# Performance work log

Measured on AMD Instinct MI355X. Metric: run time of the kernel, lower is better.

## Reference

```python
import jax, jax.numpy as jnp
import numpy as np

HEAD_DIM = 1024
SCALE = HEAD_DIM ** -0.25  # qk_scale defaults to exponent -0.25


def setup_inputs() -> dict:
    key = jax.random.key(0)
    ks = jax.random.split(key, 6)
    B_s, B_q, C = 4096, 4096, 1024
    return {
        "query": jax.random.normal(ks[0], (B_q, C), dtype=jnp.float32),
        "s": jax.random.normal(ks[1], (B_s, C), dtype=jnp.float32),
        "TG_prompt": jax.random.normal(ks[2], (B_s, C), dtype=jnp.float32),
        "W_qkv": jax.random.normal(ks[3], (3 * HEAD_DIM, C), dtype=jnp.float32) * (C ** -0.5),
        "W_proj_s": jax.random.normal(ks[4], (HEAD_DIM, HEAD_DIM), dtype=jnp.float32) * (HEAD_DIM ** -0.5),
        "W_proj_q": jax.random.normal(ks[5], (HEAD_DIM, HEAD_DIM), dtype=jnp.float32) * (HEAD_DIM ** -0.5),
    }


def reference(query, s, TG_prompt, W_qkv, W_proj_s, W_proj_q):
    B_s = s.shape[0]
    t = s + TG_prompt                       # [B_s, C]
    c = jnp.concatenate([t, query], axis=0)  # [B, C], B = B_s + B_q
    x = c @ W_qkv.T                          # [B, 3*head_dim]
    q, k, v = jnp.split(x, 3, axis=-1)       # each [B, head_dim]
    # separate sqrt-scale on q and k, then full [B, B] scores
    attn = jax.nn.softmax((q * SCALE) @ (k.T * SCALE), axis=-1)
    attn_cq = attn[:B_s, B_s:]               # [B_s, B_q]
    attn_qc = attn[B_s:, :B_s]               # [B_q, B_s]
    # matmul against raw query / s (NOT v), then per-branch projection
    x_s = (attn_cq @ query) @ W_proj_s.T     # [B_s, head_dim]
    x_q = (attn_qc @ s) @ W_proj_q.T         # [B_q, head_dim]
    return (x_s, x_q)
```

## Files before the change

kernel.cpp:

```cpp
#include <hip/hip_runtime.h>


typedef unsigned short u16;
typedef __bf16 bf16x8 __attribute__((ext_vector_type(8)));
typedef float f32x4 __attribute__((ext_vector_type(4)));
typedef unsigned short u16x8 __attribute__((ext_vector_type(8)));

#define DEVI static __device__ __forceinline__

DEVI u16 f2b(float f) {
  unsigned int u = __float_as_uint(f);
  u += 0x7fffu + ((u >> 16) & 1u);
  return (u16)(u >> 16);
}

DEVI float exp2_hw(float x) {
  float r;
  asm("v_exp_f32 %0, %1" : "=v"(r) : "v"(x));
  return r;
}

__global__ void prep_all(const float* __restrict__ query, const float* __restrict__ s,
                         const float* __restrict__ tg, const float* __restrict__ w0,
                         const float* __restrict__ w1, const float* __restrict__ w2,
                         u16* __restrict__ cB, u16* __restrict__ sBf,
                         u16* __restrict__ o0, u16* __restrict__ o1,
                         u16* __restrict__ o2, float* __restrict__ rowsum) {
  int b = blockIdx.x;
  if (b >= 6144) {
    int i = (b - 6144) * 1024 + (int)threadIdx.x * 4;
    rowsum[i] = 0.f; rowsum[i + 1] = 0.f; rowsum[i + 2] = 0.f; rowsum[i + 3] = 0.f;
    return;
  }
  if (b < 4096) {
    int base = (b * 256 + threadIdx.x) << 3;
    int row = base >> 10;
    u16x8 o;
    if (row < 4096) {
      float4 a0 = *(const float4*)(s + base);
      float4 a1 = *(const float4*)(s + base + 4);
      float4 b0 = *(const float4*)(tg + base);
      float4 b1 = *(const float4*)(tg + base + 4);
      u16x8 os;
      os[0] = f2b(a0.x); os[1] = f2b(a0.y); os[2] = f2b(a0.z); os[3] = f2b(a0.w);
      os[4] = f2b(a1.x); os[5] = f2b(a1.y); os[6] = f2b(a1.z); os[7] = f2b(a1.w);
      *(u16x8*)(sBf + base) = os;
      o[0] = f2b(a0.x + b0.x); o[1] = f2b(a0.y + b0.y);
      o[2] = f2b(a0.z + b0.z); o[3] = f2b(a0.w + b0.w);
      o[4] = f2b(a1.x + b1.x); o[5] = f2b(a1.y + b1.y);
      o[6] = f2b(a1.z + b1.z); o[7] = f2b(a1.w + b1.w);
    } else {
      int qb = base - 4096 * 1024;
      float4 a0 = *(const float4*)(query + qb);
      float4 a1 = *(const float4*)(query + qb + 4);
      o[0] = f2b(a0.x); o[1] = f2b(a0.y); o[2] = f2b(a0.z); o[3] = f2b(a0.w);
      o[4] = f2b(a1.x); o[5] = f2b(a1.y); o[6] = f2b(a1.z); o[7] = f2b(a1.w);
    }
    *(u16x8*)(cB + base) = o;
  } else {
    const float* in; u16* out; int lb;
    if (b < 5120)      { in = w0; out = o0; lb = b - 4096; }
    else if (b < 5632) { in = w1; out = o1; lb = b - 5120; }
    else               { in = w2; out = o2; lb = b - 5632; }
    int base = (lb * 256 + threadIdx.x) << 3;
    float4 a0 = *(const float4*)(in + base);
    float4 a1 = *(const float4*)(in + base + 4);
    u16x8 o;
    o[0] = f2b(a0.x); o[1] = f2b(a0.y); o[2] = f2b(a0.z); o[3] = f2b(a0.w);
    o[4] = f2b(a1.x); o[5] = f2b(a1.y); o[6] = f2b(a1.z); o[7] = f2b(a1.w);
    *(u16x8*)(out + base) = o;
  }
}

struct KLoopOut { f32x4 acc[4][4]; };

DEVI void kloop(const u16* Ab, const u16* Bb, int lda, int ldb, int K,
                u16* sA, u16* sB, int tid, int wr, int wc, f32x4 (&acc)[4][4]) {
  const int lane = tid & 63;
  const int ar = lane & 15;
  const int sr = tid >> 3;
  const int scL = (tid & 7) << 3;
  const int scG = ((tid & 7) ^ (sr & 7)) << 3;

  const int l7 = lane & 7, l16 = lane >> 4;
  const int p0b = (l16 ^ l7) << 4;
  const int offA0 = (wr + ar) * 128 + p0b;
  const int offB0 = (wc + ar) * 128 + p0b;
  const char* sAc = (const char*)sA;
  const char* sBc = (const char*)sB;

  for (int k0 = 0; k0 < K; k0 += 64) {
#pragma unroll
    for (int it = 0; it < 4; ++it) {
      int r = it * 64 + sr;
      __builtin_amdgcn_global_load_lds(
          (__attribute__((address_space(1))) void*)(Ab + (size_t)r * lda + k0 + scG),
          (__attribute__((address_space(3))) void*)(sA + r * 64 + scL), 16, 0, 0);
    }
#pragma unroll
    for (int it = 0; it < 2; ++it) {
      int r = it * 64 + sr;
      __builtin_amdgcn_global_load_lds(
          (__attribute__((address_space(1))) void*)(Bb + (size_t)r * ldb + k0 + scG),
          (__attribute__((address_space(3))) void*)(sB + r * 64 + scL), 16, 0, 0);
    }
    __syncthreads();
#pragma unroll
    for (int half = 0; half < 2; ++half) {
      const int px = half ? 64 : 0;
      bf16x8 af[4], bfr[4];
#pragma unroll
      for (int t = 0; t < 4; ++t)
        af[t] = *(const bf16x8*)(sAc + ((offA0 ^ px) + t * 2048));
#pragma unroll
      for (int t = 0; t < 4; ++t)
        bfr[t] = *(const bf16x8*)(sBc + ((offB0 ^ px) + t * 2048));
#pragma unroll
      for (int tm = 0; tm < 4; ++tm)
#pragma unroll
        for (int tn = 0; tn < 4; ++tn)
          acc[tm][tn] = __builtin_amdgcn_mfma_f32_16x16x32_bf16(
              af[tm], bfr[tn], acc[tm][tn], 0, 0, 0);
    }
    __syncthreads();
  }
}

__global__ __launch_bounds__(512)
void gemm_qkv(const u16* __restrict__ cB, const u16* __restrict__ WqkB,
              u16* __restrict__ qks,
              const u16* __restrict__ WpsB, const u16* __restrict__ WpqB,
              const u16* __restrict__ qBf, const u16* __restrict__ sBf,
              u16* __restrict__ VsT, u16* __restrict__ VqT,
              float sq, float sk) {
  __shared__ __align__(16) u16 sA[256 * 64];
  __shared__ __align__(16) u16 sB[128 * 64];
  const int b = blockIdx.x;
  const u16* Ap; const u16* Bp; u16* op;
  int bx, by, ldc;
  bool proj;
  if (b < 512) {
    proj = true;  bx = b & 15; by = b >> 4;
    Ap = cB; Bp = WqkB; op = qks; ldc = 2048;
  } else {
    proj = false;
    int b2 = b - 512;
    int z = b2 >> 7, rem = b2 & 127;
    bx = rem & 31; by = rem >> 5;
    Ap = z ? WpqB : WpsB; Bp = z ? sBf : qBf; op = z ? VqT : VsT; ldc = 4096;
  }
  const int tid = threadIdx.x;
  const int lane = tid & 63;
  const int wave = tid >> 6;
  const int wr = (wave >> 1) * 64;
  const int wc = (wave & 1) * 64;

  f32x4 acc[4][4];
#pragma unroll
  for (int i = 0; i < 4; ++i)
#pragma unroll
    for (int j = 0; j < 4; ++j) acc[i][j] = f32x4{0.f, 0.f, 0.f, 0.f};

  kloop(Ap + (size_t)(by * 256) * 1024, Bp + (size_t)(bx * 128) * 1024,
        1024, 1024, 1024, sA, sB, tid, wr, wc, acc);

  const int qr = (lane >> 4) * 4;
  const int qc = lane & 15;
#pragma unroll
  for (int tm = 0; tm < 4; ++tm)
#pragma unroll
    for (int r = 0; r < 4; ++r) {
      int row = by * 256 + wr + tm * 16 + qr + r;
#pragma unroll
      for (int tn = 0; tn < 4; ++tn) {
        int col = bx * 128 + wc + tn * 16 + qc;
        float sc = proj ? ((col < 1024) ? sq : sk) : 1.0f;
        op[(size_t)row * ldc + col] = f2b(acc[tm][tn][r] * sc);
      }
    }
}

template <int EPI>
__global__ __launch_bounds__(512)
void gemm_bt(const u16* __restrict__ A, const u16* __restrict__ A1,
             const u16* __restrict__ B, const u16* __restrict__ B1,
             int lda, int ldb, int K, int ldc,
             float* __restrict__ outf, float* __restrict__ outf1,
             const float* __restrict__ rs, const float* __restrict__ rs1,
             u16* __restrict__ Pcq, u16* __restrict__ Pqc,
             float* __restrict__ rowsum) {
  __shared__ __align__(16) u16 sA[256 * 64];
  __shared__ __align__(16) u16 sB[128 * 64];
  const int tid = threadIdx.x;
  const int lane = tid & 63;
  const int wave = tid >> 6;
  const int wr = (wave >> 1) * 64;
  const int wc = (wave & 1) * 64;
  const int by = blockIdx.y, bx = blockIdx.x;
  const int z = blockIdx.z;

  f32x4 acc[4][4];
#pragma unroll
  for (int i = 0; i < 4; ++i)
#pragma unroll
    for (int j = 0; j < 4; ++j) acc[i][j] = f32x4{0.f, 0.f, 0.f, 0.f};

  kloop((z ? A1 : A) + (size_t)(by * 256) * lda,
        (z ? B1 : B) + (size_t)(bx * 128) * ldb,
        lda, ldb, K, sA, sB, tid, wr, wc, acc);

  const int qr = (lane >> 4) * 4;
  const int qc = lane & 15;

  if constexpr (EPI == 1) {
    const bool top = (by < 16);
    const bool left = (bx < 32);
    u16* pdst = nullptr;
    if (top && !left) pdst = Pcq;
    if (!top && left) pdst = Pqc;
    const int growb = by * 256 + wr;
    const int rbase = growb - (top ? 0 : 4096);
    const int cbase = bx * 128 + wc - (left ? 0 : 4096);
#pragma unroll
    for (int tm = 0; tm < 4; ++tm) {
      float e[4][4];
      float rsum[4] = {0.f, 0.f, 0.f, 0.f};
#pragma unroll
      for (int tn = 0; tn < 4; ++tn)
#pragma unroll
        for (int r = 0; r < 4; ++r) {
          e[tn][r] = exp2_hw(acc[tm][tn][r]);
          rsum[r] += e[tn][r];
        }
#pragma unroll
      for (int r = 0; r < 4; ++r) {
        float v = rsum[r];
        v += __shfl_xor(v, 1);
        v += __shfl_xor(v, 2);
        v += __shfl_xor(v, 4);
        v += __shfl_xor(v, 8);
        if ((lane & 15) == 0)
          atomicAdd(&rowsum[growb + tm * 16 + qr + r], v);
      }
      if (pdst) {
#pragma unroll
        for (int tn = 0; tn < 4; ++tn)
#pragma unroll
          for (int r = 0; r < 4; ++r) {
            int row = rbase + tm * 16 + qr + r;
            pdst[(size_t)row * 4096 + cbase + tn * 16 + qc] = f2b(e[tn][r]);
          }
      }
    }
  } else {
    float* of = z ? outf1 : outf;
    const float* rsz = z ? rs1 : rs;
#pragma unroll
    for (int tm = 0; tm < 4; ++tm)
#pragma unroll
      for (int r = 0; r < 4; ++r) {
        int row = by * 256 + wr + tm * 16 + qr + r;
        float inv = 1.0f / rsz[row];
#pragma unroll
        for (int tn = 0; tn < 4; ++tn) {
          int col = bx * 128 + wc + tn * 16 + qc;
          of[(size_t)row * ldc + col] = acc[tm][tn][r] * inv;
        }
      }
  }
}


extern "C" void kernel_launch(void* const* d_in, const int* in_sizes, int n_in,
                              void* d_out, int out_size, void* d_ws, size_t ws_size,
                              hipStream_t stream) {
  (void)in_sizes; (void)n_in; (void)out_size; (void)ws_size;
  const float* query = (const float*)d_in[0];
  const float* s     = (const float*)d_in[1];
  const float* tg    = (const float*)d_in[2];
  const float* Wqkv  = (const float*)d_in[3];
  const float* Wps   = (const float*)d_in[4];
  const float* Wpq   = (const float*)d_in[5];
  float* out = (float*)d_out;

  char* ws = (char*)d_ws;
  u16* cB     = (u16*)ws; ws += (size_t)8192 * 1024 * 2;
  u16* sBf    = (u16*)ws; ws += (size_t)4096 * 1024 * 2;
  u16* qks    = (u16*)ws; ws += (size_t)8192 * 2048 * 2;
  u16* WqkB   = (u16*)ws; ws += (size_t)2048 * 1024 * 2;
  u16* WpsB   = (u16*)ws; ws += (size_t)1024 * 1024 * 2;
  u16* WpqB   = (u16*)ws; ws += (size_t)1024 * 1024 * 2;
  u16* VsT    = (u16*)ws; ws += (size_t)1024 * 4096 * 2;
  u16* VqT    = (u16*)ws; ws += (size_t)1024 * 4096 * 2;
  u16* Pcq    = (u16*)ws; ws += (size_t)4096 * 4096 * 2;
  u16* Pqc    = (u16*)ws; ws += (size_t)4096 * 4096 * 2;
  float* rowsum = (float*)ws;

  const u16* qBf = cB + (size_t)4096 * 1024;

  const float SCALE = 0.17677669529663687f;
  const float LOG2E = 1.4426950408889634f;

  prep_all<<<6152, 256, 0, stream>>>(query, s, tg, Wqkv, Wps, Wpq,
                                     cB, sBf, WqkB, WpsB, WpqB, rowsum);
  gemm_qkv<<<768, 512, 0, stream>>>(cB, WqkB, qks, WpsB, WpqB, qBf, sBf,
                                    VsT, VqT, SCALE * LOG2E, SCALE);
  gemm_bt<1><<<dim3(64, 32), 512, 0, stream>>>(
      qks, nullptr, qks + 1024, nullptr, 2048, 2048, 1024, 0,
      nullptr, nullptr, nullptr, nullptr, Pcq, Pqc, rowsum);
  gemm_bt<4><<<dim3(8, 16, 2), 512, 0, stream>>>(
      Pcq, Pqc, VsT, VqT, 4096, 4096, 4096, 1024,
      out, out + (size_t)4096 * 1024, rowsum, rowsum + 4096,
      nullptr, nullptr, nullptr);
}
```

Measured before the change: 431.0 us.

## Replace score GEMM with 256x256-tile double-buffered kernel using direct-to-LDS loads

Adds a dedicated scores kernel that uses 256x256 output tiles per block instead of 256x128. Tiles are staged through global_load_lds into double-buffered LDS, with MFMA groups split into quarters separated by barriers and raised wave priority. This raises arithmetic intensity and overlaps the next K-tile's loads with compute for the dominant 8192x8192x1024 GEMM. In exchange it doubles the accumulator registers per thread (acc[8][4]), uses 128KB of LDS, and halves the grid, which may lower occupancy.

```diff
diff --git a/kernel.cpp b/kernel.cpp
--- a/kernel.cpp
+++ b/kernel.cpp
@@ -72,8 +72,6 @@
   }
 }
 
-struct KLoopOut { f32x4 acc[4][4]; };
-
 DEVI void kloop(const u16* Ab, const u16* Bb, int lda, int ldb, int K,
                 u16* sA, u16* sB, int tid, int wr, int wc, f32x4 (&acc)[4][4]) {
   const int lane = tid & 63;
@@ -180,6 +178,167 @@
     }
 }
 
+__global__ __launch_bounds__(512)
+void gemm_sc(const u16* __restrict__ A, const u16* __restrict__ B,
+             u16* __restrict__ Pcq, u16* __restrict__ Pqc,
+             float* __restrict__ rowsum) {
+  __shared__ __align__(16) u16 lds[2][2][256 * 64];
+  const int tid = threadIdx.x;
+  const int lane = tid & 63;
+  const int wave = tid >> 6;
+  const int wm = wave >> 2;
+  const int wn = wave & 3;
+  const int bx = blockIdx.x, by = blockIdx.y;
+
+  const int sr = tid >> 3;
+  const int scL = (tid & 7) << 3;
+  const int scG = ((tid & 7) ^ (sr & 7)) << 3;
+
+  const int l7 = lane & 7, l16 = lane >> 4;
+  const int ar = lane & 15;
+  const int p0b = (l16 ^ l7) << 4;
+  const int offA0 = (wm * 128 + ar) * 128 + p0b;
+  const int offB0 = (wn * 64 + ar) * 128 + p0b;
+
+  const u16* Ag = A + (size_t)(by * 256) * 2048;
+  const u16* Bg = B + (size_t)(bx * 256) * 2048;
+
+#define STAGE_SC(DST, K0)                                                     \
+  _Pragma("unroll")                                                           \
+  for (int it_ = 0; it_ < 4; ++it_) {                                         \
+    const int r_ = it_ * 64 + sr;                                             \
+    __builtin_amdgcn_global_load_lds(                                         \
+        (__attribute__((address_space(1))) void*)(Ag + (size_t)r_ * 2048 + (K0) + scG), \
+        (__attribute__((address_space(3))) void*)(&lds[DST][0][r_ * 64 + scL]), 16, 0, 0); \
+    __builtin_amdgcn_global_load_lds(                                         \
+        (__attribute__((address_space(1))) void*)(Bg + (size_t)r_ * 2048 + (K0) + scG), \
+        (__attribute__((address_space(3))) void*)(&lds[DST][1][r_ * 64 + scL]), 16, 0, 0); \
+  }
+
+#define MFMA_Q(MQ, NQ)                                                        \
+  _Pragma("unroll")                                                           \
+  for (int tm_ = 0; tm_ < 4; ++tm_) {                                         \
+    _Pragma("unroll")                                                         \
+    for (int tn_ = 0; tn_ < 2; ++tn_) {                                       \
+      _Pragma("unroll")                                                       \
+      for (int kh_ = 0; kh_ < 2; ++kh_)                                       \
+        acc[(MQ) * 4 + tm_][(NQ) * 2 + tn_] =                                 \
+            __builtin_amdgcn_mfma_f32_16x16x32_bf16(                          \
+                af[tm_][kh_], bfr[NQ][tn_][kh_],                              \
+                acc[(MQ) * 4 + tm_][(NQ) * 2 + tn_], 0, 0, 0);                \
+    }                                                                         \
+  }
+
+  f32x4 acc[8][4];
+#pragma unroll
+  for (int i = 0; i < 8; ++i)
+#pragma unroll
+    for (int j = 0; j < 4; ++j) acc[i][j] = f32x4{0.f, 0.f, 0.f, 0.f};
+
+  STAGE_SC(0, 0)
+
+#pragma unroll 1
+  for (int kt = 0; kt < 16; ++kt) {
+    const int cur = kt & 1;
+    const char* sAc = (const char*)lds[cur][0];
+    const char* sBc = (const char*)lds[cur][1];
+
+    if (kt < 15) {
+      STAGE_SC(cur ^ 1, (kt + 1) * 64)
+      asm volatile("s_waitcnt vmcnt(8)\n\ts_barrier" ::: "memory");
+    } else {
+      asm volatile("s_waitcnt vmcnt(0)\n\ts_barrier" ::: "memory");
+    }
+
+    bf16x8 af[4][2];
+    bf16x8 bfr[2][2][2];
+#pragma unroll
+    for (int t_ = 0; t_ < 4; ++t_) {
+      af[t_][0] = *(const bf16x8*)(sAc + (offA0 + t_ * 2048));
+      af[t_][1] = *(const bf16x8*)(sAc + ((offA0 + t_ * 2048) ^ 64));
+    }
+#pragma unroll
+    for (int nq_ = 0; nq_ < 2; ++nq_)
+#pragma unroll
+      for (int t_ = 0; t_ < 2; ++t_) {
+        bfr[nq_][t_][0] = *(const bf16x8*)(sBc + (offB0 + nq_ * 4096 + t_ * 2048));
+        bfr[nq_][t_][1] = *(const bf16x8*)(sBc + ((offB0 + nq_ * 4096 + t_ * 2048) ^ 64));
+      }
+    asm volatile("s_waitcnt lgkmcnt(0)" ::: "memory");
+    __builtin_amdgcn_sched_barrier(0);
+    __builtin_amdgcn_s_setprio(1);
+    MFMA_Q(0, 0)
+    __builtin_amdgcn_s_setprio(0);
+    asm volatile("s_barrier" ::: "memory");
+
+    __builtin_amdgcn_s_setprio(1);
+    MFMA_Q(0, 1)
+    __builtin_amdgcn_s_setprio(0);
+    asm volatile("s_barrier" ::: "memory");
+
+#pragma unroll
+    for (int t_ = 0; t_ < 4; ++t_) {
+      af[t_][0] = *(const bf16x8*)(sAc + (offA0 + 8192 + t_ * 2048));
+      af[t_][1] = *(const bf16x8*)(sAc + ((offA0 + 8192 + t_ * 2048) ^ 64));
+    }
+    asm volatile("s_waitcnt lgkmcnt(0)" ::: "memory");
+    __builtin_amdgcn_sched_barrier(0);
+    __builtin_amdgcn_s_setprio(1);
+    MFMA_Q(1, 0)
+    __builtin_amdgcn_s_setprio(0);
+    asm volatile("s_barrier" ::: "memory");
+
+    __builtin_amdgcn_s_setprio(1);
+    MFMA_Q(1, 1)
+    __builtin_amdgcn_s_setprio(0);
+    asm volatile("s_barrier" ::: "memory");
+  }
+
+  const int qr = (lane >> 4) * 4;
+  const int qc = lane & 15;
+  const bool top = (by < 16);
+  const bool left = (bx < 16);
+  u16* pdst = nullptr;
+  if (top && !left) pdst = Pcq;
+  if (!top && left) pdst = Pqc;
+  const int growb = by * 256 + wm * 128;
+  const int rbase = growb - (top ? 0 : 4096);
+  const int cbase = bx * 256 + wn * 64 - (left ? 0 : 4096);
+#pragma unroll
+  for (int i = 0; i < 8; ++i) {
+    float e[4][4];
+    float rsum[4] = {0.f, 0.f, 0.f, 0.f};
+#pragma unroll
+    for (int j = 0; j < 4; ++j)
+#pragma unroll
+      for (int r = 0; r < 4; ++r) {
+        e[j][r] = exp2_hw(acc[i][j][r]);
+        rsum[r] += e[j][r];
+      }
+#pragma unroll
+    for (int r = 0; r < 4; ++r) {
+      float v = rsum[r];
+      v += __shfl_xor(v, 1);
+      v += __shfl_xor(v, 2);
+      v += __shfl_xor(v, 4);
+      v += __shfl_xor(v, 8);
+      if ((lane & 15) == 0)
+        atomicAdd(&rowsum[growb + i * 16 + qr + r], v);
+    }
+    if (pdst) {
+#pragma unroll
+      for (int j = 0; j < 4; ++j)
+#pragma unroll
+        for (int r = 0; r < 4; ++r) {
+          int row = rbase + i * 16 + qr + r;
+          pdst[(size_t)row * 4096 + cbase + j * 16 + qc] = f2b(e[j][r]);
+        }
+    }
+  }
+#undef STAGE_SC
+#undef MFMA_Q
+}
+
 template <int EPI>
 __global__ __launch_bounds__(512)
 void gemm_bt(const u16* __restrict__ A, const u16* __restrict__ A1,
@@ -212,47 +371,7 @@
   const int qr = (lane >> 4) * 4;
   const int qc = lane & 15;
 
-  if constexpr (EPI == 1) {
-    const bool top = (by < 16);
-    const bool left = (bx < 32);
-    u16* pdst = nullptr;
-    if (top && !left) pdst = Pcq;
-    if (!top && left) pdst = Pqc;
-    const int growb = by * 256 + wr;
-    const int rbase = growb - (top ? 0 : 4096);
-    const int cbase = bx * 128 + wc - (left ? 0 : 4096);
-#pragma unroll
-    for (int tm = 0; tm < 4; ++tm) {
-      float e[4][4];
-      float rsum[4] = {0.f, 0.f, 0.f, 0.f};
-#pragma unroll
-      for (int tn = 0; tn < 4; ++tn)
-#pragma unroll
-        for (int r = 0; r < 4; ++r) {
-          e[tn][r] = exp2_hw(acc[tm][tn][r]);
-          rsum[r] += e[tn][r];
-        }
-#pragma unroll
-      for (int r = 0; r < 4; ++r) {
-        float v = rsum[r];
-        v += __shfl_xor(v, 1);
-        v += __shfl_xor(v, 2);
-        v += __shfl_xor(v, 4);
-        v += __shfl_xor(v, 8);
-        if ((lane & 15) == 0)
-          atomicAdd(&rowsum[growb + tm * 16 + qr + r], v);
-      }
-      if (pdst) {
-#pragma unroll
-        for (int tn = 0; tn < 4; ++tn)
-#pragma unroll
-          for (int r = 0; r < 4; ++r) {
-            int row = rbase + tm * 16 + qr + r;
-            pdst[(size_t)row * 4096 + cbase + tn * 16 + qc] = f2b(e[tn][r]);
-          }
-      }
-    }
-  } else {
+  if constexpr (EPI == 4) {
     float* of = z ? outf1 : outf;
     const float* rsz = z ? rs1 : rs;
 #pragma unroll
@@ -305,9 +424,7 @@
                                      cB, sBf, WqkB, WpsB, WpqB, rowsum);
   gemm_qkv<<<768, 512, 0, stream>>>(cB, WqkB, qks, WpsB, WpqB, qBf, sBf,
                                     VsT, VqT, SCALE * LOG2E, SCALE);
-  gemm_bt<1><<<dim3(64, 32), 512, 0, stream>>>(
-      qks, nullptr, qks + 1024, nullptr, 2048, 2048, 1024, 0,
-      nullptr, nullptr, nullptr, nullptr, Pcq, Pqc, rowsum);
+  gemm_sc<<<dim3(32, 32), 512, 0, stream>>>(qks, qks + 1024, Pcq, Pqc, rowsum);
   gemm_bt<4><<<dim3(8, 16, 2), 512, 0, stream>>>(
       Pcq, Pqc, VsT, VqT, 4096, 4096, 4096, 1024,
       out, out + (size_t)4096 * 1024, rowsum, rowsum + 4096,
```

New measurement: 448.0 us. 1.04x slower.

## Swizzle block order across XCDs and use smaller 128x128 tiles for PV GEMM

Applied to the files above, without the earlier changes.

Remaps linear block indices in the QKV and scores GEMMs so consecutive blocks scheduled on the same XCD share neighbouring tiles, with the aim of improving L2 reuse. The final PV GEMM moves from 256x128 tiles (256 blocks) to 128x128 tiles with 256 threads (512 blocks), which gives more blocks to fill the GPU's CUs. The cost is more redundant loads of the B operand and fewer waves per block to hide latency in the PV stage.

```diff
diff --git a/kernel.cpp b/kernel.cpp
--- a/kernel.cpp
+++ b/kernel.cpp
@@ -72,8 +72,6 @@
   }
 }
 
-struct KLoopOut { f32x4 acc[4][4]; };
-
 DEVI void kloop(const u16* Ab, const u16* Bb, int lda, int ldb, int K,
                 u16* sA, u16* sB, int tid, int wr, int wc, f32x4 (&acc)[4][4]) {
   const int lane = tid & 63;
@@ -100,6 +98,58 @@
 #pragma unroll
     for (int it = 0; it < 2; ++it) {
       int r = it * 64 + sr;
+      __builtin_amdgcn_global_load_lds(
+          (__attribute__((address_space(1))) void*)(Bb + (size_t)r * ldb + k0 + scG),
+          (__attribute__((address_space(3))) void*)(sB + r * 64 + scL), 16, 0, 0);
+    }
+    __syncthreads();
+#pragma unroll
+    for (int half = 0; half < 2; ++half) {
+      const int px = half ? 64 : 0;
+      bf16x8 af[4], bfr[4];
+#pragma unroll
+      for (int t = 0; t < 4; ++t)
+        af[t] = *(const bf16x8*)(sAc + ((offA0 ^ px) + t * 2048));
+#pragma unroll
+      for (int t = 0; t < 4; ++t)
+        bfr[t] = *(const bf16x8*)(sBc + ((offB0 ^ px) + t * 2048));
+#pragma unroll
+      for (int tm = 0; tm < 4; ++tm)
+#pragma unroll
+        for (int tn = 0; tn < 4; ++tn)
+          acc[tm][tn] = __builtin_amdgcn_mfma_f32_16x16x32_bf16(
+              af[tm], bfr[tn], acc[tm][tn], 0, 0, 0);
+    }
+    __syncthreads();
+  }
+}
+
+DEVI void kloop128(const u16* Ab, const u16* Bb, int lda, int ldb, int K,
+                   u16* sA, u16* sB, int tid, int wr, int wc, f32x4 (&acc)[4][4]) {
+  const int lane = tid & 63;
+  const int ar = lane & 15;
+  const int sr = tid >> 3;
+  const int scL = (tid & 7) << 3;
+  const int scG = ((tid & 7) ^ (sr & 7)) << 3;
+
+  const int l7 = lane & 7, l16 = lane >> 4;
+  const int p0b = (l16 ^ l7) << 4;
+  const int offA0 = (wr + ar) * 128 + p0b;
+  const int offB0 = (wc + ar) * 128 + p0b;
+  const char* sAc = (const char*)sA;
+  const char* sBc = (const char*)sB;
+
+  for (int k0 = 0; k0 < K; k0 += 64) {
+#pragma unroll
+    for (int it = 0; it < 4; ++it) {
+      int r = it * 32 + sr;
+      __builtin_amdgcn_global_load_lds(
+          (__attribute__((address_space(1))) void*)(Ab + (size_t)r * lda + k0 + scG),
+          (__attribute__((address_space(3))) void*)(sA + r * 64 + scL), 16, 0, 0);
+    }
+#pragma unroll
+    for (int it = 0; it < 4; ++it) {
+      int r = it * 32 + sr;
       __builtin_amdgcn_global_load_lds(
           (__attribute__((address_space(1))) void*)(Bb + (size_t)r * ldb + k0 + scG),
           (__attribute__((address_space(3))) void*)(sB + r * 64 + scL), 16, 0, 0);
@@ -135,7 +185,8 @@
               float sq, float sk) {
   __shared__ __align__(16) u16 sA[256 * 64];
   __shared__ __align__(16) u16 sB[128 * 64];
-  const int b = blockIdx.x;
+  int b = blockIdx.x;
+  b = (b & 7) * 96 + (b >> 3);
   const u16* Ap; const u16* Bp; u16* op;
   int bx, by, ldc;
   bool proj;
@@ -180,15 +231,9 @@
     }
 }
 
-template <int EPI>
 __global__ __launch_bounds__(512)
-void gemm_bt(const u16* __restrict__ A, const u16* __restrict__ A1,
-             const u16* __restrict__ B, const u16* __restrict__ B1,
-             int lda, int ldb, int K, int ldc,
-             float* __restrict__ outf, float* __restrict__ outf1,
-             const float* __restrict__ rs, const float* __restrict__ rs1,
-             u16* __restrict__ Pcq, u16* __restrict__ Pqc,
-             float* __restrict__ rowsum) {
+void gemm_scores(const u16* __restrict__ qks, u16* __restrict__ Pcq,
+                 u16* __restrict__ Pqc, float* __restrict__ rowsum) {
   __shared__ __align__(16) u16 sA[256 * 64];
   __shared__ __align__(16) u16 sB[128 * 64];
   const int tid = threadIdx.x;
@@ -196,8 +241,10 @@
   const int wave = tid >> 6;
   const int wr = (wave >> 1) * 64;
   const int wc = (wave & 1) * 64;
-  const int by = blockIdx.y, bx = blockIdx.x;
-  const int z = blockIdx.z;
+  int b = blockIdx.x;
+  int swz = (b & 7) * 256 + (b >> 3);
+  const int bx = swz & 63;
+  const int by = swz >> 6;
 
   f32x4 acc[4][4];
 #pragma unroll
@@ -205,69 +252,98 @@
 #pragma unroll
     for (int j = 0; j < 4; ++j) acc[i][j] = f32x4{0.f, 0.f, 0.f, 0.f};
 
-  kloop((z ? A1 : A) + (size_t)(by * 256) * lda,
-        (z ? B1 : B) + (size_t)(bx * 128) * ldb,
-        lda, ldb, K, sA, sB, tid, wr, wc, acc);
+  kloop(qks + (size_t)(by * 256) * 2048,
+        qks + 1024 + (size_t)(bx * 128) * 2048,
+        2048, 2048, 1024, sA, sB, tid, wr, wc, acc);
 
   const int qr = (lane >> 4) * 4;
   const int qc = lane & 15;
-
-  if constexpr (EPI == 1) {
-    const bool top = (by < 16);
-    const bool left = (bx < 32);
-    u16* pdst = nullptr;
-    if (top && !left) pdst = Pcq;
-    if (!top && left) pdst = Pqc;
-    const int growb = by * 256 + wr;
-    const int rbase = growb - (top ? 0 : 4096);
-    const int cbase = bx * 128 + wc - (left ? 0 : 4096);
-#pragma unroll
-    for (int tm = 0; tm < 4; ++tm) {
-      float e[4][4];
-      float rsum[4] = {0.f, 0.f, 0.f, 0.f};
+  const bool top = (by < 16);
+  const bool left = (bx < 32);
+  u16* pdst = nullptr;
+  if (top && !left) pdst = Pcq;
+  if (!top && left) pdst = Pqc;
+  const int growb = by * 256 + wr;
+  const int rbase = growb - (top ? 0 : 4096);
+  const int cbase = bx * 128 + wc - (left ? 0 : 4096);
+#pragma unroll
+  for (int tm = 0; tm < 4; ++tm) {
+    float e[4][4];
+    float rsum[4] = {0.f, 0.f, 0.f, 0.f};
+#pragma unroll
+    for (int tn = 0; tn < 4; ++tn)
+#pragma unroll
+      for (int r = 0; r < 4; ++r) {
+        e[tn][r] = exp2_hw(acc[tm][tn][r]);
+        rsum[r] += e[tn][r];
+      }
+#pragma unroll
+    for (int r = 0; r < 4; ++r) {
+      float v = rsum[r];
+      v += __shfl_xor(v, 1);
+      v += __shfl_xor(v, 2);
+      v += __shfl_xor(v, 4);
+      v += __shfl_xor(v, 8);
+      if ((lane & 15) == 0)
+        atomicAdd(&rowsum[growb + tm * 16 + qr + r], v);
+    }
+    if (pdst) {
 #pragma unroll
       for (int tn = 0; tn < 4; ++tn)
 #pragma unroll
         for (int r = 0; r < 4; ++r) {
-          e[tn][r] = exp2_hw(acc[tm][tn][r]);
-          rsum[r] += e[tn][r];
+          int row = rbase + tm * 16 + qr + r;
+          pdst[(size_t)row * 4096 + cbase + tn * 16 + qc] = f2b(e[tn][r]);
         }
-#pragma unroll
-      for (int r = 0; r < 4; ++r) {
-        float v = rsum[r];
-        v += __shfl_xor(v, 1);
-        v += __shfl_xor(v, 2);
-        v += __shfl_xor(v, 4);
-        v += __shfl_xor(v, 8);
-        if ((lane & 15) == 0)
-          atomicAdd(&rowsum[growb + tm * 16 + qr + r], v);
+    }
+  }
+}
+
+__global__ __launch_bounds__(256)
+void gemm_pv(const u16* __restrict__ Pcq, const u16* __restrict__ Pqc,
+             const u16* __restrict__ VsT, const u16* __restrict__ VqT,
+             const float* __restrict__ rowsum,
+             float* __restrict__ out0, float* __restrict__ out1) {
+  __shared__ __align__(16) u16 sA[128 * 64];
+  __shared__ __align__(16) u16 sB[128 * 64];
+  const int tid = threadIdx.x;
+  const int lane = tid & 63;
+  const int wave = tid >> 6;
+  const int wr = (wave >> 1) * 64;
+  const int wc = (wave & 1) * 64;
+  int b = blockIdx.x;
+  int swz = (b & 7) * 64 + (b >> 3);
+  const int z = swz >> 8;
+  const int rem = swz & 255;
+  const int by = rem >> 3;
+  const int bx = rem & 7;
+
+  f32x4 acc[4][4];
+#pragma unroll
+  for (int i = 0; i < 4; ++i)
+#pragma unroll
+    for (int j = 0; j < 4; ++j) acc[i][j] = f32x4{0.f, 0.f, 0.f, 0.f};
+
+  kloop128((z ? Pqc : Pcq) + (size_t)(by * 128) * 4096,
+           (z ? VqT : VsT) + (size_t)(bx * 128) * 4096,
+           4096, 4096, 4096, sA, sB, tid, wr, wc, acc);
+
+  const int qr = (lane >> 4) * 4;
+  const int qc = lane & 15;
+  float* of = z ? out1 : out0;
+  const float* rsz = rowsum + z * 4096;
+#pragma unroll
+  for (int tm = 0; tm < 4; ++tm)
+#pragma unroll
+    for (int r = 0; r < 4; ++r) {
+      int row = by * 128 + wr + tm * 16 + qr + r;
+      float inv = 1.0f / rsz[row];
+#pragma unroll
+      for (int tn = 0; tn < 4; ++tn) {
+        int col = bx * 128 + wc + tn * 16 + qc;
+        of[(size_t)row * 1024 + col] = acc[tm][tn][r] * inv;
       }
-      if (pdst) {
-#pragma unroll
-        for (int tn = 0; tn < 4; ++tn)
-#pragma unroll
-          for (int r = 0; r < 4; ++r) {
-            int row = rbase + tm * 16 + qr + r;
-            pdst[(size_t)row * 4096 + cbase + tn * 16 + qc] = f2b(e[tn][r]);
-          }
-      }
-    }
-  } else {
-    float* of = z ? outf1 : outf;
-    const float* rsz = z ? rs1 : rs;
-#pragma unroll
-    for (int tm = 0; tm < 4; ++tm)
-#pragma unroll
-      for (int r = 0; r < 4; ++r) {
-        int row = by * 256 + wr + tm * 16 + qr + r;
-        float inv = 1.0f / rsz[row];
-#pragma unroll
-        for (int tn = 0; tn < 4; ++tn) {
-          int col = bx * 128 + wc + tn * 16 + qc;
-          of[(size_t)row * ldc + col] = acc[tm][tn][r] * inv;
-        }
-      }
-  }
+    }
 }
 
 
@@ -305,11 +381,7 @@
                                      cB, sBf, WqkB, WpsB, WpqB, rowsum);
   gemm_qkv<<<768, 512, 0, stream>>>(cB, WqkB, qks, WpsB, WpqB, qBf, sBf,
                                     VsT, VqT, SCALE * LOG2E, SCALE);
-  gemm_bt<1><<<dim3(64, 32), 512, 0, stream>>>(
-      qks, nullptr, qks + 1024, nullptr, 2048, 2048, 1024, 0,
-      nullptr, nullptr, nullptr, nullptr, Pcq, Pqc, rowsum);
-  gemm_bt<4><<<dim3(8, 16, 2), 512, 0, stream>>>(
-      Pcq, Pqc, VsT, VqT, 4096, 4096, 4096, 1024,
-      out, out + (size_t)4096 * 1024, rowsum, rowsum + 4096,
-      nullptr, nullptr, nullptr);
-}
+  gemm_scores<<<2048, 512, 0, stream>>>(qks, Pcq, Pqc, rowsum);
+  gemm_pv<<<512, 256, 0, stream>>>(Pcq, Pqc, VsT, VqT, rowsum,
+                                   out, out + (size_t)4096 * 1024);
+}
```

Measured after the change: 421.1 us. 1.02x faster.
